# Performance work log

Measured on AMD Instinct MI355X. Metric: run time of the kernel, lower is better.

## Reference

```python
import jax, jax.numpy as jnp
import numpy as np

T, B, I, H = 512, 64, 512, 512

def setup_inputs() -> dict:
    key = jax.random.key(0)
    k1, k2, k3 = jax.random.split(key, 3)
    # scale weights to keep tanh out of deep saturation
    return {
        "input": jax.random.normal(k1, (T, B, I), dtype=jnp.float32),
        "w_ih": jax.random.normal(k2, (H, I), dtype=jnp.float32) / np.sqrt(I),
        "w_hh": jax.random.normal(k3, (H, H), dtype=jnp.float32) / np.sqrt(H),
    }

def reference(input, w_ih, w_hh):
    # vanilla tanh RNN: h_t = tanh(x_t @ w_ih^T + h_{t-1} @ w_hh^T)
    batch = input.shape[1]
    h0 = jnp.zeros((batch, w_hh.shape[0]), dtype=input.dtype)

    def step(h_prev, x):
        h = jnp.tanh(x @ w_ih.T + h_prev @ w_hh.T)
        return h, h

    h_last, h_all = jax.lax.scan(step, h0, input)
    return h_all, h_last
```

## Files before the change

kernel.cpp:

```cpp
#include <hip/hip_runtime.h>
#include <cmath>

#define T_STEPS 512
#define BATCH   64
#define ISZ     512
#define HSZ     512
#define EXN     32768

__device__ __forceinline__ void ex_store(unsigned long long* w, float h, unsigned tag) {
    union { float f; unsigned u; } c; c.f = h;
    const unsigned long long v = ((unsigned long long)tag << 32) | (unsigned long long)c.u;
    __hip_atomic_store(w, v, __ATOMIC_RELAXED, __HIP_MEMORY_SCOPE_AGENT);
}

__device__ __forceinline__ float4 ld_pin_f4(const float* p) {
    float4 v;
    asm volatile("global_load_dwordx4 %0, %1, off" : "=v"(v) : "v"(p));
    return v;
}

__device__ __forceinline__ float dot16_fold(const float4 (&W)[4][4],
                                            const float4* __restrict__ src,
                                            int parbase4, int kseg) {
    const float4* s0 = src + parbase4 + kseg * 5;
    const float4* s1 = s0 + 160;
    float A0 = 0.f, A1 = 0.f, A2 = 0.f, A3 = 0.f;
    float B0 = 0.f, B1 = 0.f, B2 = 0.f, B3 = 0.f;
    #pragma unroll
    for (int i = 0; i < 4; ++i) {
        const float4 h0 = s0[i];
        const float4 h1 = s1[i];
        const float4 w0 = W[0][i], w1 = W[1][i], w2 = W[2][i], w3 = W[3][i];
        A0 = fmaf(w0.x, h0.x, A0); A0 = fmaf(w0.y, h0.y, A0);
        A0 = fmaf(w0.z, h0.z, A0); A0 = fmaf(w0.w, h0.w, A0);
        A1 = fmaf(w1.x, h0.x, A1); A1 = fmaf(w1.y, h0.y, A1);
        A1 = fmaf(w1.z, h0.z, A1); A1 = fmaf(w1.w, h0.w, A1);
        A2 = fmaf(w2.x, h0.x, A2); A2 = fmaf(w2.y, h0.y, A2);
        A2 = fmaf(w2.z, h0.z, A2); A2 = fmaf(w2.w, h0.w, A2);
        A3 = fmaf(w3.x, h0.x, A3); A3 = fmaf(w3.y, h0.y, A3);
        A3 = fmaf(w3.z, h0.z, A3); A3 = fmaf(w3.w, h0.w, A3);
        B0 = fmaf(w0.x, h1.x, B0); B0 = fmaf(w0.y, h1.y, B0);
        B0 = fmaf(w0.z, h1.z, B0); B0 = fmaf(w0.w, h1.w, B0);
        B1 = fmaf(w1.x, h1.x, B1); B1 = fmaf(w1.y, h1.y, B1);
        B1 = fmaf(w1.z, h1.z, B1); B1 = fmaf(w1.w, h1.w, B1);
        B2 = fmaf(w2.x, h1.x, B2); B2 = fmaf(w2.y, h1.y, B2);
        B2 = fmaf(w2.z, h1.z, B2); B2 = fmaf(w2.w, h1.w, B2);
        B3 = fmaf(w3.x, h1.x, B3); B3 = fmaf(w3.y, h1.y, B3);
        B3 = fmaf(w3.z, h1.z, B3); B3 = fmaf(w3.w, h1.w, B3);
    }
    const bool sb0 = (kseg & 1) != 0;
    const bool sb1 = (kseg & 2) != 0;
    const bool sb2 = (kseg & 4) != 0;
    const float u0 = (sb0 ? B0 : A0) + __shfl_xor(sb0 ? A0 : B0, 1, 64);
    const float u1 = (sb0 ? B1 : A1) + __shfl_xor(sb0 ? A1 : B1, 1, 64);
    const float u2 = (sb0 ? B2 : A2) + __shfl_xor(sb0 ? A2 : B2, 1, 64);
    const float u3 = (sb0 ? B3 : A3) + __shfl_xor(sb0 ? A3 : B3, 1, 64);
    const float w01 = (sb1 ? u1 : u0) + __shfl_xor(sb1 ? u0 : u1, 2, 64);
    const float w23 = (sb1 ? u3 : u2) + __shfl_xor(sb1 ? u2 : u3, 2, 64);
    float z = (sb2 ? w23 : w01) + __shfl_xor(sb2 ? w01 : w23, 4, 64);
    z += __shfl_xor(z, 8, 64);
    z += __shfl_xor(z, 16, 64);
    return z;
}

__global__ __launch_bounds__(512, 2) void rnn_fused(const float* __restrict__ x,
                                                    const float* __restrict__ wih,
                                                    const float* __restrict__ whh,
                                                    float* __restrict__ out,
                                                    unsigned long long* __restrict__ ex) {
    __shared__ __align__(16) float hls[2560];
    __shared__ __align__(16) float xss[2560];
    const float4* hl4 = (const float4*)hls;
    const float4* xs4 = (const float4*)xss;

    const int tid  = threadIdx.x;
    const int bid  = blockIdx.x;
    const int xcd  = bid & 7;
    const int ib   = bid >> 3;
    const int p    = xcd * 4 + (ib & 3);
    const int g    = ib >> 2;
    const int kseg = tid & 31;
    const int jg   = tid >> 5;
    const int jb   = g * 64 + jg * 4;

    float4 wh[4][4], wi[4][4];
    #pragma unroll
    for (int r = 0; r < 4; ++r) {
        const float* hr = whh + (size_t)(jb + r) * HSZ + kseg * 16;
        const float* ir = wih + (size_t)(jb + r) * ISZ + kseg * 16;
        #pragma unroll
        for (int i = 0; i < 4; ++i) {
            wh[r][i] = ld_pin_f4(hr + 4 * i);
            wi[r][i] = ld_pin_f4(ir + 4 * i);
        }
    }
    asm volatile("s_waitcnt vmcnt(0)" ::: "memory");
    __builtin_amdgcn_sched_barrier(0);

    unsigned long long* exw0 = ex + (size_t)(2 * p + 0) * 512 + tid;
    unsigned long long* exw1 = ex + (size_t)(2 * p + 1) * 512 + tid;

    const int whf = (tid >> 4) * 20 + ((tid >> 2) & 3) * 4 + (tid & 3);

    const int bx = tid >> 8;
    const int io = (tid & 255) * 2;
    const int xf = bx * 640 + (io >> 4) * 20 + ((io >> 2) & 3) * 4 + (io & 3);
    const float* xsrc = x + (size_t)(2 * p + bx) * ISZ + io;

    const int row  = ((kseg >> 1) & 1) + 2 * ((kseg >> 2) & 1);
    const int br   = kseg & 1;
    const int outj = jb + row;
    const int outb = 2 * p + br;
    float* outp = out + (size_t)outb * HSZ + outj;
    unsigned long long* exself = ex + (size_t)outb * 512 + outj;

    {
        const float2 v = *(const float2*)xsrc;
        *(float2*)&xss[xf] = v;
    }
    __syncthreads();
    float xwv = dot16_fold(wi, xs4, 0, kseg);

    for (int t = 0; t < T_STEPS; ++t) {
        const int  parh4 = (t & 1) * 320;
        const bool havex = (t < T_STEPS - 1);

        float2 xv;
        if (havex) xv = *(const float2*)(xsrc + (size_t)(t + 1) * (BATCH * ISZ));

        if (t > 0) {
            const size_t soff = (size_t)((t - 1) & 1) * EXN;
            unsigned long long v0 = __hip_atomic_load(exw0 + soff, __ATOMIC_RELAXED,
                                                      __HIP_MEMORY_SCOPE_AGENT);
            unsigned long long v1 = __hip_atomic_load(exw1 + soff, __ATOMIC_RELAXED,
                                                      __HIP_MEMORY_SCOPE_AGENT);
            while ((unsigned)(v0 >> 32) != (unsigned)t ||
                   (unsigned)(v1 >> 32) != (unsigned)t) {
                __builtin_amdgcn_s_sleep(1);
                v0 = __hip_atomic_load(exw0 + soff, __ATOMIC_RELAXED,
                                       __HIP_MEMORY_SCOPE_AGENT);
                v1 = __hip_atomic_load(exw1 + soff, __ATOMIC_RELAXED,
                                       __HIP_MEMORY_SCOPE_AGENT);
            }
            union { unsigned u; float f; } c0, c1;
            c0.u = (unsigned)v0; c1.u = (unsigned)v1;
            hls[parh4 * 4 + whf]       = c0.f;
            hls[parh4 * 4 + 640 + whf] = c1.f;
        }
        if (havex) *(float2*)&xss[((t + 1) & 1) * 1280 + xf] = xv;
        __syncthreads();

        float acc = 0.f;
        if (t > 0)
            acc = dot16_fold(wh, hl4, parh4, kseg);

        if (kseg < 8) {
            const float a2 = acc + xwv;
            const float e  = __expf(2.f * a2);
            const float hv = 1.f - 2.f / (e + 1.f);
            outp[(size_t)t * (BATCH * HSZ)] = hv;
            if (havex)
                ex_store(exself + (size_t)(t & 1) * EXN, hv, (unsigned)(t + 1));
            else
                out[(size_t)T_STEPS * BATCH * HSZ + (size_t)outb * HSZ + outj] = hv;
        }

        if (havex)
            xwv = dot16_fold(wi, xs4, ((t + 1) & 1) * 320, kseg);
    }
}

extern "C" void kernel_launch(void* const* d_in, const int* in_sizes, int n_in,
                              void* d_out, int out_size, void* d_ws, size_t ws_size,
                              hipStream_t stream) {
    (void)in_sizes; (void)n_in; (void)out_size; (void)ws_size;
    const float* x   = (const float*)d_in[0];
    const float* wih = (const float*)d_in[1];
    const float* whh = (const float*)d_in[2];
    float*       out = (float*)d_out;
    unsigned long long* ex = (unsigned long long*)d_ws;

    (void)hipMemsetAsync(d_ws, 0, 2 * EXN * sizeof(unsigned long long), stream);

    hipLaunchKernelGGL(rnn_fused, dim3(256), dim3(512), 0, stream,
                       x, wih, whh, out, ex);
}
```

Before: 1.020 ms.

## Split RNN work across twice as many smaller blocks; publish hidden state before output store

Launches 512 blocks of 256 threads instead of 256 blocks of 512, so each block owns 32 hidden units instead of 64. Each thread now polls four exchange slots and loads x with float4 instead of float2. The goal is to spread the recurrent dot products over more CUs and cut per-block work on the critical path. The exchange store is also moved ahead of the output write so other blocks see the new state sooner. In exchange, twice as many blocks spin on the flag-based exchange each step, which adds global polling traffic and synchronisation overhead.

```diff
diff --git a/kernel.cpp b/kernel.cpp
--- a/kernel.cpp
+++ b/kernel.cpp
@@ -63,7 +63,7 @@
     return z;
 }
 
-__global__ __launch_bounds__(512, 2) void rnn_fused(const float* __restrict__ x,
+__global__ __launch_bounds__(256, 2) void rnn_fused(const float* __restrict__ x,
                                                     const float* __restrict__ wih,
                                                     const float* __restrict__ whh,
                                                     float* __restrict__ out,
@@ -81,7 +81,7 @@
     const int g    = ib >> 2;
     const int kseg = tid & 31;
     const int jg   = tid >> 5;
-    const int jb   = g * 64 + jg * 4;
+    const int jb   = g * 32 + jg * 4;
 
     float4 wh[4][4], wi[4][4];
     #pragma unroll
@@ -97,15 +97,17 @@
     asm volatile("s_waitcnt vmcnt(0)" ::: "memory");
     __builtin_amdgcn_sched_barrier(0);
 
-    unsigned long long* exw0 = ex + (size_t)(2 * p + 0) * 512 + tid;
-    unsigned long long* exw1 = ex + (size_t)(2 * p + 1) * 512 + tid;
+    unsigned long long* ex00 = ex + (size_t)(2 * p + 0) * 512 + tid;
+    unsigned long long* ex01 = ex00 + 256;
+    unsigned long long* ex10 = ex + (size_t)(2 * p + 1) * 512 + tid;
+    unsigned long long* ex11 = ex10 + 256;
 
     const int whf = (tid >> 4) * 20 + ((tid >> 2) & 3) * 4 + (tid & 3);
 
-    const int bx = tid >> 8;
-    const int io = (tid & 255) * 2;
-    const int xf = bx * 640 + (io >> 4) * 20 + ((io >> 2) & 3) * 4 + (io & 3);
-    const float* xsrc = x + (size_t)(2 * p + bx) * ISZ + io;
+    const int bx  = tid >> 7;
+    const int idx = tid & 127;
+    const int xf4 = bx * 160 + (idx >> 2) * 5 + (idx & 3);
+    const float* xsrc = x + (size_t)(2 * p + bx) * ISZ + idx * 4;
 
     const int row  = ((kseg >> 1) & 1) + 2 * ((kseg >> 2) & 1);
     const int br   = kseg & 1;
@@ -114,10 +116,7 @@
     float* outp = out + (size_t)outb * HSZ + outj;
     unsigned long long* exself = ex + (size_t)outb * 512 + outj;
 
-    {
-        const float2 v = *(const float2*)xsrc;
-        *(float2*)&xss[xf] = v;
-    }
+    ((float4*)xss)[xf4] = *(const float4*)xsrc;
     __syncthreads();
     float xwv = dot16_fold(wi, xs4, 0, kseg);
 
@@ -125,29 +124,40 @@
         const int  parh4 = (t & 1) * 320;
         const bool havex = (t < T_STEPS - 1);
 
-        float2 xv;
-        if (havex) xv = *(const float2*)(xsrc + (size_t)(t + 1) * (BATCH * ISZ));
+        float4 xv;
+        if (havex) xv = *(const float4*)(xsrc + (size_t)(t + 1) * (BATCH * ISZ));
 
         if (t > 0) {
             const size_t soff = (size_t)((t - 1) & 1) * EXN;
-            unsigned long long v0 = __hip_atomic_load(exw0 + soff, __ATOMIC_RELAXED,
-                                                      __HIP_MEMORY_SCOPE_AGENT);
-            unsigned long long v1 = __hip_atomic_load(exw1 + soff, __ATOMIC_RELAXED,
-                                                      __HIP_MEMORY_SCOPE_AGENT);
-            while ((unsigned)(v0 >> 32) != (unsigned)t ||
-                   (unsigned)(v1 >> 32) != (unsigned)t) {
+            unsigned long long v00 = __hip_atomic_load(ex00 + soff, __ATOMIC_RELAXED,
+                                                       __HIP_MEMORY_SCOPE_AGENT);
+            unsigned long long v01 = __hip_atomic_load(ex01 + soff, __ATOMIC_RELAXED,
+                                                       __HIP_MEMORY_SCOPE_AGENT);
+            unsigned long long v10 = __hip_atomic_load(ex10 + soff, __ATOMIC_RELAXED,
+                                                       __HIP_MEMORY_SCOPE_AGENT);
+            unsigned long long v11 = __hip_atomic_load(ex11 + soff, __ATOMIC_RELAXED,
+                                                       __HIP_MEMORY_SCOPE_AGENT);
+            while ((unsigned)(v00 >> 32) != (unsigned)t ||
+                   (unsigned)(v01 >> 32) != (unsigned)t ||
+                   (unsigned)(v10 >> 32) != (unsigned)t ||
+                   (unsigned)(v11 >> 32) != (unsigned)t) {
                 __builtin_amdgcn_s_sleep(1);
-                v0 = __hip_atomic_load(exw0 + soff, __ATOMIC_RELAXED,
-                                       __HIP_MEMORY_SCOPE_AGENT);
-                v1 = __hip_atomic_load(exw1 + soff, __ATOMIC_RELAXED,
-                                       __HIP_MEMORY_SCOPE_AGENT);
+                v00 = __hip_atomic_load(ex00 + soff, __ATOMIC_RELAXED,
+                                        __HIP_MEMORY_SCOPE_AGENT);
+                v01 = __hip_atomic_load(ex01 + soff, __ATOMIC_RELAXED,
+                                        __HIP_MEMORY_SCOPE_AGENT);
+                v10 = __hip_atomic_load(ex10 + soff, __ATOMIC_RELAXED,
+                                        __HIP_MEMORY_SCOPE_AGENT);
+                v11 = __hip_atomic_load(ex11 + soff, __ATOMIC_RELAXED,
+                                        __HIP_MEMORY_SCOPE_AGENT);
             }
-            union { unsigned u; float f; } c0, c1;
-            c0.u = (unsigned)v0; c1.u = (unsigned)v1;
-            hls[parh4 * 4 + whf]       = c0.f;
-            hls[parh4 * 4 + 640 + whf] = c1.f;
+            union { unsigned u; float f; } c;
+            c.u = (unsigned)v00; hls[parh4 * 4 + whf]             = c.f;
+            c.u = (unsigned)v01; hls[parh4 * 4 + whf + 320]       = c.f;
+            c.u = (unsigned)v10; hls[parh4 * 4 + 640 + whf]       = c.f;
+            c.u = (unsigned)v11; hls[parh4 * 4 + 640 + whf + 320] = c.f;
         }
-        if (havex) *(float2*)&xss[((t + 1) & 1) * 1280 + xf] = xv;
+        if (havex) ((float4*)xss)[((t + 1) & 1) * 320 + xf4] = xv;
         __syncthreads();
 
         float acc = 0.f;
@@ -158,10 +168,10 @@
             const float a2 = acc + xwv;
             const float e  = __expf(2.f * a2);
             const float hv = 1.f - 2.f / (e + 1.f);
-            outp[(size_t)t * (BATCH * HSZ)] = hv;
             if (havex)
                 ex_store(exself + (size_t)(t & 1) * EXN, hv, (unsigned)(t + 1));
-            else
+            outp[(size_t)t * (BATCH * HSZ)] = hv;
+            if (!havex)
                 out[(size_t)T_STEPS * BATCH * HSZ + (size_t)outb * HSZ + outj] = hv;
         }
 
@@ -182,6 +192,6 @@
 
     (void)hipMemsetAsync(d_ws, 0, 2 * EXN * sizeof(unsigned long long), stream);
 
-    hipLaunchKernelGGL(rnn_fused, dim3(256), dim3(512), 0, stream,
+    hipLaunchKernelGGL(rnn_fused, dim3(512), dim3(256), 0, stream,
                        x, wih, whh, out, ex);
 }
```

Measured after the change: 1.049 ms. +2.8%, slower.

## Add fast-path sc0 polling with dual exchange buffers and fallback slow path

Applied to the files above, without the earlier changes.

Each producer now writes its tagged hidden value twice: once with a plain sc0 store to a fast buffer and once with an agent-scope atomic store to a separate slow buffer. Consumers first spin up to 20 times on the fast buffer with sc0 loads and no sleep. If that fails, they permanently fall back to sleeping atomic polling on the slow buffer. The exchange store is also moved ahead of the output store. The aim is lower cross-block handoff latency per timestep, at the cost of doubled exchange writes and a coherence path that is only safe because of the fallback.

```diff
diff --git a/kernel.cpp b/kernel.cpp
--- a/kernel.cpp
+++ b/kernel.cpp
@@ -7,10 +7,13 @@
 #define HSZ     512
 #define EXN     32768
 
-__device__ __forceinline__ void ex_store(unsigned long long* w, float h, unsigned tag) {
+__device__ __forceinline__ void ex_store_dual(unsigned long long* wf,
+                                              unsigned long long* ws,
+                                              float h, unsigned tag) {
     union { float f; unsigned u; } c; c.f = h;
     const unsigned long long v = ((unsigned long long)tag << 32) | (unsigned long long)c.u;
-    __hip_atomic_store(w, v, __ATOMIC_RELAXED, __HIP_MEMORY_SCOPE_AGENT);
+    asm volatile("global_store_dwordx2 %0, %1, off sc0" :: "v"(wf), "v"(v) : "memory");
+    __hip_atomic_store(ws, v, __ATOMIC_RELAXED, __HIP_MEMORY_SCOPE_AGENT);
 }
 
 __device__ __forceinline__ float4 ld_pin_f4(const float* p) {
@@ -97,8 +100,8 @@
     asm volatile("s_waitcnt vmcnt(0)" ::: "memory");
     __builtin_amdgcn_sched_barrier(0);
 
-    unsigned long long* exw0 = ex + (size_t)(2 * p + 0) * 512 + tid;
-    unsigned long long* exw1 = ex + (size_t)(2 * p + 1) * 512 + tid;
+    unsigned long long* exf0 = ex + (size_t)(2 * p + 0) * 512 + tid;
+    unsigned long long* exf1 = ex + (size_t)(2 * p + 1) * 512 + tid;
 
     const int whf = (tid >> 4) * 20 + ((tid >> 2) & 3) * 4 + (tid & 3);
 
@@ -112,7 +115,8 @@
     const int outj = jb + row;
     const int outb = 2 * p + br;
     float* outp = out + (size_t)outb * HSZ + outj;
-    unsigned long long* exself = ex + (size_t)outb * 512 + outj;
+    unsigned long long* exfself = ex + (size_t)outb * 512 + outj;
+    unsigned long long* exsself = exfself + 2 * (size_t)EXN;
 
     {
         const float2 v = *(const float2*)xsrc;
@@ -121,6 +125,8 @@
     __syncthreads();
     float xwv = dot16_fold(wi, xs4, 0, kseg);
 
+    int fastm = 1;
+
     for (int t = 0; t < T_STEPS; ++t) {
         const int  parh4 = (t & 1) * 320;
         const bool havex = (t < T_STEPS - 1);
@@ -130,17 +136,38 @@
 
         if (t > 0) {
             const size_t soff = (size_t)((t - 1) & 1) * EXN;
-            unsigned long long v0 = __hip_atomic_load(exw0 + soff, __ATOMIC_RELAXED,
-                                                      __HIP_MEMORY_SCOPE_AGENT);
-            unsigned long long v1 = __hip_atomic_load(exw1 + soff, __ATOMIC_RELAXED,
-                                                      __HIP_MEMORY_SCOPE_AGENT);
-            while ((unsigned)(v0 >> 32) != (unsigned)t ||
-                   (unsigned)(v1 >> 32) != (unsigned)t) {
-                __builtin_amdgcn_s_sleep(1);
-                v0 = __hip_atomic_load(exw0 + soff, __ATOMIC_RELAXED,
-                                       __HIP_MEMORY_SCOPE_AGENT);
-                v1 = __hip_atomic_load(exw1 + soff, __ATOMIC_RELAXED,
-                                       __HIP_MEMORY_SCOPE_AGENT);
+            const unsigned long long* f0 = exf0 + soff;
+            const unsigned long long* f1 = exf1 + soff;
+            unsigned long long v0 = 0, v1 = 0;
+            bool ok0 = false, ok1 = false;
+
+            if (fastm) {
+                for (int k = 0; k < 20; ++k) {
+                    unsigned long long a, b;
+                    asm volatile(
+                        "global_load_dwordx2 %0, %2, off sc0\n\t"
+                        "global_load_dwordx2 %1, %3, off sc0\n\t"
+                        "s_waitcnt vmcnt(0)"
+                        : "=&v"(a), "=&v"(b) : "v"(f0), "v"(f1) : "memory");
+                    if (!ok0 && (unsigned)(a >> 32) == (unsigned)t) { v0 = a; ok0 = true; }
+                    if (!ok1 && (unsigned)(b >> 32) == (unsigned)t) { v1 = b; ok1 = true; }
+                    if (ok0 && ok1) break;
+                }
+                if (!(ok0 && ok1)) fastm = 0;
+            }
+            if (!(ok0 && ok1)) {
+                const unsigned long long* s0 = f0 + 2 * (size_t)EXN;
+                const unsigned long long* s1 = f1 + 2 * (size_t)EXN;
+                for (;;) {
+                    unsigned long long c = __hip_atomic_load(s0, __ATOMIC_RELAXED,
+                                                             __HIP_MEMORY_SCOPE_AGENT);
+                    unsigned long long d = __hip_atomic_load(s1, __ATOMIC_RELAXED,
+                                                             __HIP_MEMORY_SCOPE_AGENT);
+                    if (!ok0 && (unsigned)(c >> 32) == (unsigned)t) { v0 = c; ok0 = true; }
+                    if (!ok1 && (unsigned)(d >> 32) == (unsigned)t) { v1 = d; ok1 = true; }
+                    if (ok0 && ok1) break;
+                    __builtin_amdgcn_s_sleep(1);
+                }
             }
             union { unsigned u; float f; } c0, c1;
             c0.u = (unsigned)v0; c1.u = (unsigned)v1;
@@ -158,10 +185,12 @@
             const float a2 = acc + xwv;
             const float e  = __expf(2.f * a2);
             const float hv = 1.f - 2.f / (e + 1.f);
+            if (havex) {
+                const size_t so = (size_t)(t & 1) * EXN;
+                ex_store_dual(exfself + so, exsself + so, hv, (unsigned)(t + 1));
+            }
             outp[(size_t)t * (BATCH * HSZ)] = hv;
-            if (havex)
-                ex_store(exself + (size_t)(t & 1) * EXN, hv, (unsigned)(t + 1));
-            else
+            if (!havex)
                 out[(size_t)T_STEPS * BATCH * HSZ + (size_t)outb * HSZ + outj] = hv;
         }
 
@@ -180,7 +209,7 @@
     float*       out = (float*)d_out;
     unsigned long long* ex = (unsigned long long*)d_ws;
 
-    (void)hipMemsetAsync(d_ws, 0, 2 * EXN * sizeof(unsigned long long), stream);
+    (void)hipMemsetAsync(d_ws, 0, 4 * EXN * sizeof(unsigned long long), stream);
 
     hipLaunchKernelGGL(rnn_fused, dim3(256), dim3(512), 0, stream,
                        x, wih, whh, out, ex);
```

Measured after the change: 1.272 ms. +24.7%, slower.
